# Optimization experiments

Measured on AMD Instinct MI355X. Metric: run time of the kernel, lower is better.

## Reference

```python
import jax, jax.numpy as jnp
import numpy as np
import math

B, S, D, H, R = 4, 2048, 512, 8, 8  # R = k+1 relative slots per direction


def setup_inputs() -> dict:
    key = jax.random.key(0)
    ks = jax.random.split(key, 16)
    dk = D // H
    sc = 1.0 / math.sqrt(D)
    return {
        "query": jax.random.normal(ks[0], (B, S, D), jnp.float32),
        "key": jax.random.normal(ks[1], (B, S, D), jnp.float32),
        "value": jax.random.normal(ks[2], (B, S, D), jnp.float32),
        "start_nodes": jax.random.randint(ks[3], (B, H, R, S), 0, S, jnp.int64 if jax.config.jax_enable_x64 else jnp.int32),
        "end_nodes": jax.random.randint(ks[4], (B, H, R, S), 0, S, jnp.int64 if jax.config.jax_enable_x64 else jnp.int32),
        "rel_q": jax.random.normal(ks[5], (1, H, 2 * R, dk), jnp.float32),
        "rel_k": jax.random.normal(ks[6], (1, H, 2 * R, dk), jnp.float32),
        "rel_v": jax.random.normal(ks[7], (1, H, 2 * R, dk), jnp.float32),
        "Wq": jax.random.normal(ks[8], (D, D), jnp.float32) * sc,
        "bq": jnp.zeros((D,), jnp.float32),
        "Wk": jax.random.normal(ks[9], (D, D), jnp.float32) * sc,
        "bk": jnp.zeros((D,), jnp.float32),
        "Wv": jax.random.normal(ks[10], (D, D), jnp.float32) * sc,
        "bv": jnp.zeros((D,), jnp.float32),
        "Wo": jax.random.normal(ks[11], (D, D), jnp.float32) * sc,
        "bo": jnp.zeros((D,), jnp.float32),
    }


def reference(query, key, value, start_nodes, end_nodes, rel_q, rel_k, rel_v,
              Wq, bq, Wk, bk, Wv, bv, Wo, bo):
    Bs, Ss, Ds = query.shape
    Hs = start_nodes.shape[1]
    dk = Ds // Hs

    def proj(x, W, b):
        return (x @ W.T + b).reshape(Bs, Ss, Hs, dk).transpose(0, 2, 1, 3)  # [B,H,S,dk]

    q = proj(query, Wq, bq)
    k = proj(key, Wk, bk)
    v = proj(value, Wv, bv)

    start_mask = start_nodes == -1
    sn = jnp.where(start_mask, 0, start_nodes)  # -1 padding -> 0 (masked out below)
    qidx = jnp.concatenate([end_nodes, sn], axis=2)  # [B,H,2R,S]
    kidx = jnp.concatenate([sn, end_nodes], axis=2)

    bi = jnp.arange(Bs)[:, None, None, None]
    hi = jnp.arange(Hs)[None, :, None, None]
    q_ctx = q[bi, hi, qidx]  # [B,H,2R,S,dk]
    k_ctx = k[bi, hi, kidx]
    v_ctx = v[bi, hi, kidx]

    # c2c + c2p + p2c, scale_factor = 3 (rel_q and rel_k both provided)
    scores = ((q_ctx * k_ctx).sum(-1)
              + (q_ctx * rel_k[:, :, :, None, :]).sum(-1)
              + (rel_q[:, :, :, None, :] * k_ctx).sum(-1))
    scores = scores / (3.0 * jnp.sqrt(jnp.asarray(dk, scores.dtype)))

    # mask: padded edges masked in both halves; first S flat entries always masked
    mask = jnp.concatenate([start_mask, start_mask], axis=2).reshape(Bs, Hs, -1)
    mask = mask.at[:, :, :Ss].set(True)
    sflat = jnp.exp(jnp.where(mask, -1e9, scores.reshape(Bs, Hs, -1)))  # [B,H,2R*S]

    qf = qidx.reshape(Bs, Hs, -1)
    b2 = jnp.arange(Bs)[:, None, None]
    h2 = jnp.arange(Hs)[None, :, None]
    # scatter-add softmax denominator over destination nodes, then gather back
    denom = jnp.zeros((Bs, Hs, Ss), sflat.dtype).at[b2, h2, qf].add(sflat)
    denom = jnp.where(denom == 0, -1e9, denom)
    probs = (sflat / denom[b2, h2, qf]).reshape(Bs, Hs, -1, Ss, 1)  # [B,H,2R,S,1]

    attn_v = probs * (v_ctx + rel_v[:, :, :, None, :])  # [B,H,2R,S,dk]
    out = jnp.zeros((Bs, Hs, Ss, dk), attn_v.dtype).at[b2, h2, qf].add(
        attn_v.reshape(Bs, Hs, -1, dk))  # scatter-add aggregation over edges

    out = out.transpose(0, 2, 1, 3).reshape(Bs, Ss, Ds)
    return out @ Wo.T + bo
```

## Files before the change

kernel.cpp:

```cpp
#include <hip/hip_runtime.h>
#include <math.h>

#define B_ 4
#define S_ 2048
#define D_ 512
#define H_ 8
#define R_ 8
#define DK_ 64
#define NEDGE (B_*H_*2*R_*S_)
#define EPB   (2*R_*S_)
#define ELLCAP 64

typedef __attribute__((ext_vector_type(8))) short bf16x8;
typedef __attribute__((ext_vector_type(8))) unsigned short ushort8_t;
typedef __attribute__((ext_vector_type(4))) float f32x4;

#define AS1q const __attribute__((address_space(1)))
#define AS3q __attribute__((address_space(3)))

__device__ inline unsigned short f2bf(float f) {
    unsigned u = __builtin_bit_cast(unsigned, f);
    u += 0x7fffu + ((u >> 16) & 1u);
    return (unsigned short)(u >> 16);
}
__device__ inline float bf2f(unsigned short u) {
    return __builtin_bit_cast(float, ((unsigned)u) << 16);
}

__global__ __launch_bounds__(256) void prep(
    const float* __restrict__ query, const float* __restrict__ key,
    const float* __restrict__ value,
    const float* __restrict__ Wq, const float* __restrict__ Wk,
    const float* __restrict__ Wv, const float* __restrict__ Wo,
    const float* __restrict__ rel_q, const float* __restrict__ rel_k,
    const float* __restrict__ rel_v,
    unsigned short* __restrict__ qc, unsigned short* __restrict__ kc,
    unsigned short* __restrict__ vc,
    unsigned short* __restrict__ wqb, unsigned short* __restrict__ wkb,
    unsigned short* __restrict__ wvb, unsigned short* __restrict__ wob,
    unsigned short* __restrict__ rqb, unsigned short* __restrict__ rkb,
    unsigned short* __restrict__ rvb)
{
    int bid = blockIdx.x;
    const float* x;
    unsigned short* y;
    size_t i;
    if (bid < 12288) {
        int z = bid >> 12;
        x = (z == 0) ? query : (z == 1) ? key : value;
        y = (z == 0) ? qc : (z == 1) ? kc : vc;
        i = ((size_t)(bid & 4095) * 256 + threadIdx.x) * 4;
    } else if (bid < 13312) {
        int r = bid - 12288;
        int z = r >> 8;
        x = (z == 0) ? Wq : (z == 1) ? Wk : (z == 2) ? Wv : Wo;
        y = (z == 0) ? wqb : (z == 1) ? wkb : (z == 2) ? wvb : wob;
        i = ((size_t)(r & 255) * 256 + threadIdx.x) * 4;
    } else {
        int r = bid - 13312;
        int z = r >> 3;
        x = (z == 0) ? rel_q : (z == 1) ? rel_k : rel_v;
        y = (z == 0) ? rqb : (z == 1) ? rkb : rvb;
        i = ((size_t)(r & 7) * 256 + threadIdx.x) * 4;
    }
    float4 v = *(const float4*)&x[i];
    *(ushort4*)&y[i] = make_ushort4(f2bf(v.x), f2bf(v.y), f2bf(v.z), f2bf(v.w));
}

template<int TN>
__global__ __launch_bounds__(256) void gemm_bf16(
    const unsigned short* __restrict__ A0, const unsigned short* __restrict__ A1,
    const unsigned short* __restrict__ A2,
    const unsigned short* __restrict__ W0, const unsigned short* __restrict__ W1,
    const unsigned short* __restrict__ W2,
    const float* __restrict__ bi0, const float* __restrict__ bi1, const float* __restrict__ bi2,
    unsigned short* __restrict__ C0, unsigned short* __restrict__ C1,
    unsigned short* __restrict__ C2,
    float* __restrict__ Cf, int a_bhsd)
{
    constexpr int NFR = TN / 32;
    __shared__ unsigned short As[128 * 64];
    __shared__ unsigned short Bs[TN * 64];
    const int z = blockIdx.z;
    const unsigned short* A = (z == 0) ? A0 : (z == 1) ? A1 : A2;
    const unsigned short* W = (z == 0) ? W0 : (z == 1) ? W1 : W2;
    const float* bias        = (z == 0) ? bi0 : (z == 1) ? bi1 : bi2;
    unsigned short* C        = (z == 0) ? C0 : (z == 1) ? C1 : C2;

    const int t    = threadIdx.x;
    const int lane = t & 63;
    const int w    = t >> 6;
    const int wm   = w >> 1, wn = w & 1;
    const int m0   = blockIdx.x * 128;
    const int n0   = blockIdx.y * TN;

    const int lr    = lane >> 3;
    const int cglob = (lane & 7) ^ lr;

    f32x4 acc[4][NFR] = {};

    for (int kk = 0; kk < D_; kk += 64) {
        #pragma unroll
        for (int i = 0; i < 4; ++i) {
            int rowl = w * 32 + i * 8;
            int m = m0 + rowl + lr;
            const unsigned short* ga;
            if (a_bhsd) {
                int b = m >> 11, s = m & (S_ - 1), h = kk >> 6;
                ga = A + ((((size_t)b * H_ + h) * S_ + s) << 6) + cglob * 8;
            } else {
                ga = A + (size_t)m * D_ + kk + cglob * 8;
            }
            __builtin_amdgcn_global_load_lds((AS1q unsigned*)ga,
                (AS3q unsigned*)(As + rowl * 64), 16, 0, 0);
        }
        #pragma unroll
        for (int i = 0; i < TN / 32; ++i) {
            int rowl = w * (TN / 4) + i * 8;
            const unsigned short* gb =
                W + (size_t)(n0 + rowl + lr) * D_ + kk + cglob * 8;
            __builtin_amdgcn_global_load_lds((AS1q unsigned*)gb,
                (AS3q unsigned*)(Bs + rowl * 64), 16, 0, 0);
        }
        __syncthreads();

        #pragma unroll
        for (int ks = 0; ks < 64; ks += 32) {
            const int c0 = ks >> 3;
            bf16x8 af[4], bfr[NFR];
            #pragma unroll
            for (int mi = 0; mi < 4; ++mi) {
                int row = wm * 64 + mi * 16 + (lane & 15);
                int cp  = (c0 + (lane >> 4)) ^ (lane & 7);
                af[mi] = *(const bf16x8*)&As[row * 64 + cp * 8];
            }
            #pragma unroll
            for (int nj = 0; nj < NFR; ++nj) {
                int row = wn * (TN / 2) + nj * 16 + (lane & 15);
                int cp  = (c0 + (lane >> 4)) ^ (lane & 7);
                bfr[nj] = *(const bf16x8*)&Bs[row * 64 + cp * 8];
            }
            #pragma unroll
            for (int mi = 0; mi < 4; ++mi)
                #pragma unroll
                for (int nj = 0; nj < NFR; ++nj)
                    acc[mi][nj] = __builtin_amdgcn_mfma_f32_16x16x32_bf16(af[mi], bfr[nj], acc[mi][nj], 0, 0, 0);
        }
        __syncthreads();
    }

    #pragma unroll
    for (int mi = 0; mi < 4; ++mi) {
        #pragma unroll
        for (int nj = 0; nj < NFR; ++nj) {
            #pragma unroll
            for (int r = 0; r < 4; ++r) {
                int m = m0 + wm * 64 + mi * 16 + (lane >> 4) * 4 + r;
                int n = n0 + wn * (TN / 2) + nj * 16 + (lane & 15);
                float val = acc[mi][nj][r] + bias[n];
                if (Cf) {
                    Cf[(size_t)m * D_ + n] = val;
                } else {
                    int b = m >> 11, s = m & (S_ - 1);
                    int h = n >> 6,  d = n & 63;
                    C[((((size_t)b * H_ + h) * S_ + s) << 6) + d] = f2bf(val);
                }
            }
        }
    }
}

__global__ __launch_bounds__(1024) void attn_fused(
    const unsigned short* __restrict__ q, const unsigned short* __restrict__ k_,
    const unsigned short* __restrict__ v_,
    const unsigned short* __restrict__ rel_q, const unsigned short* __restrict__ rel_k,
    const unsigned short* __restrict__ rel_v,
    const int* __restrict__ start_nodes, const int* __restrict__ end_nodes,
    unsigned short* __restrict__ attn)
{
    __shared__ unsigned short ell[128 * ELLCAP];
    __shared__ int cnt[128];
    const int bi  = blockIdx.x;
    const int xcd = bi & 7;
    const int loc = bi >> 3;
    const int bh  = xcd * 4 + (loc >> 4);
    const int dlo = (loc & 15) << 7;
    const int t   = threadIdx.x;

    if (t < 128) cnt[t] = 0;
    __syncthreads();

    const int base_idx = bh * (R_ * S_);
    for (int f = t; f < EPB; f += 1024) {
        int r2 = f >> 11;
        if (r2 == 0) continue;
        int s = f & (S_ - 1);
        int idx = base_idx + (r2 & 7) * S_ + s;
        int sn = start_nodes[idx];
        if (sn == -1) continue;
        int en = end_nodes[idx];
        int dst = (r2 < R_) ? en : sn;
        unsigned rel = (unsigned)(dst - dlo);
        if (rel < 128u) {
            int ki = (r2 < R_) ? sn : en;
            int pos = atomicAdd(&cnt[rel], 1);
            if (pos < ELLCAP)
                ell[(rel << 6) + pos] = (unsigned short)((r2 << 11) | ki);
        }
    }
    __syncthreads();

    const int w    = t >> 6;
    const int lane = t & 63;
    const int grp  = lane >> 3;
    const int sub  = lane & 7;
    const int h    = bh & 7;
    const size_t node_base = ((size_t)bh << 11);

    for (int dd = 0; dd < 8; ++dd) {
        int dl  = dd * 16 + w;
        int dst = dlo + dl;

        ushort8_t q8 = *(const ushort8_t*)&q[((node_base + dst) << 6) + sub * 8];
        float qv[8];
        #pragma unroll
        for (int i = 0; i < 8; ++i) qv[i] = bf2f(q8[i]);

        int n = cnt[dl];
        if (n > ELLCAP) n = ELLCAP;
        int d_all = (int)ell[(dl << 6) + lane];

        float den = 0.f;
        float o[8] = {};
        #pragma unroll 2
        for (int j = 0; j < n; j += 8) {
            int slot = j + grp;
            int d = __shfl(d_all, slot);
            bool valid = slot < n;
            int ki = d & (S_ - 1);
            int r2 = (d >> 11) & 15;
            ushort8_t k8  = *(const ushort8_t*)&k_  [((node_base + ki) << 6) + sub * 8];
            ushort8_t rk8 = *(const ushort8_t*)&rel_k[(((h << 4) + r2) << 6) + sub * 8];
            ushort8_t rq8 = *(const ushort8_t*)&rel_q[(((h << 4) + r2) << 6) + sub * 8];
            float p = 0.f;
            #pragma unroll
            for (int i = 0; i < 8; ++i)
                p = fmaf(bf2f(k8[i]), qv[i] + bf2f(rq8[i]),
                         fmaf(qv[i], bf2f(rk8[i]), p));
            p += __shfl_xor(p, 1);
            p += __shfl_xor(p, 2);
            p += __shfl_xor(p, 4);
            float sf = valid ? __expf(p * (1.0f / 24.0f)) : 0.f;
            ushort8_t v8  = *(const ushort8_t*)&v_  [((node_base + ki) << 6) + sub * 8];
            ushort8_t rv8 = *(const ushort8_t*)&rel_v[(((h << 4) + r2) << 6) + sub * 8];
            den += sf;
            #pragma unroll
            for (int i = 0; i < 8; ++i)
                o[i] = fmaf(sf, bf2f(v8[i]) + bf2f(rv8[i]), o[i]);
        }
        den += __shfl_xor(den, 8); den += __shfl_xor(den, 16); den += __shfl_xor(den, 32);
        #pragma unroll
        for (int i = 0; i < 8; ++i) {
            o[i] += __shfl_xor(o[i], 8);
            o[i] += __shfl_xor(o[i], 16);
            o[i] += __shfl_xor(o[i], 32);
        }
        if (grp == 0) {
            float inv = (den > 0.f) ? 1.0f / den : 0.f;
            ushort8_t r;
            #pragma unroll
            for (int i = 0; i < 8; ++i) r[i] = f2bf(o[i] * inv);
            *(ushort8_t*)&attn[((node_base + dst) << 6) + sub * 8] = r;
        }
    }
}

extern "C" void kernel_launch(void* const* d_in, const int* in_sizes, int n_in,
                              void* d_out, int out_size, void* d_ws, size_t ws_size,
                              hipStream_t stream) {
    const float* query = (const float*)d_in[0];
    const float* key   = (const float*)d_in[1];
    const float* value = (const float*)d_in[2];
    const int* start_nodes = (const int*)d_in[3];
    const int* end_nodes   = (const int*)d_in[4];
    const float* rel_q = (const float*)d_in[5];
    const float* rel_k = (const float*)d_in[6];
    const float* rel_v = (const float*)d_in[7];
    const float* Wq = (const float*)d_in[8];
    const float* bq = (const float*)d_in[9];
    const float* Wk = (const float*)d_in[10];
    const float* bk = (const float*)d_in[11];
    const float* Wv = (const float*)d_in[12];
    const float* bv = (const float*)d_in[13];
    const float* Wo = (const float*)d_in[14];
    const float* bo = (const float*)d_in[15];
    float* out = (float*)d_out;

    const size_t NQ = (size_t)B_ * H_ * S_ * DK_;
    const size_t NW = (size_t)D_ * D_;
    const size_t NR = (size_t)H_ * 2 * R_ * DK_;
    unsigned short* p = (unsigned short*)d_ws;
    unsigned short* qc = p;            p += NQ;
    unsigned short* kc = p;            p += NQ;
    unsigned short* vc = p;            p += NQ;
    unsigned short* q  = p;            p += NQ;
    unsigned short* k  = p;            p += NQ;
    unsigned short* v  = p;            p += NQ;
    unsigned short* attn = p;          p += NQ;
    unsigned short* wqb = p;           p += NW;
    unsigned short* wkb = p;           p += NW;
    unsigned short* wvb = p;           p += NW;
    unsigned short* wob = p;           p += NW;
    unsigned short* rqb = p;           p += NR;
    unsigned short* rkb = p;           p += NR;
    unsigned short* rvb = p;           p += NR;

    prep<<<13336, 256, 0, stream>>>(query, key, value, Wq, Wk, Wv, Wo,
                                    rel_q, rel_k, rel_v,
                                    qc, kc, vc, wqb, wkb, wvb, wob,
                                    rqb, rkb, rvb);

    dim3 ggrid(B_ * S_ / 128, D_ / 128, 3);
    gemm_bf16<128><<<ggrid, 256, 0, stream>>>(qc, kc, vc, wqb, wkb, wvb, bq, bk, bv,
                                              q, k, v, nullptr, 0);

    attn_fused<<<512, 1024, 0, stream>>>(q, k, v, rqb, rkb, rvb,
                                         start_nodes, end_nodes, attn);

    dim3 ogrid(B_ * S_ / 128, D_ / 64, 1);
    gemm_bf16<64><<<ogrid, 256, 0, stream>>>(attn, attn, attn, wob, wob, wob, bo, bo, bo,
                                             nullptr, nullptr, nullptr, out, 1);
}
```

Before: 217.2 us.

## Precompute per-node relative-position score terms in a separate kernel

Adds a rel_dots kernel that computes q·rel_k and k·rel_q for every node and all 16 relative slots, stores them in fp32 scratch that reuses the qc buffer, and has the attention loop read these scalars instead of recomputing two extra dot products per edge. rel_v is now read directly in fp32, and the edge-bucketing loop loads start/end node pairs as int2 and skips the always-masked first segment up front. This cuts per-edge arithmetic and rel-table loads in the gather loop. In exchange it adds a kernel launch, extra per-edge scattered scalar loads from rqk, and changes precision slightly because the rel terms are no longer rounded to bf16.

```diff
diff --git a/kernel.cpp b/kernel.cpp
--- a/kernel.cpp
+++ b/kernel.cpp
@@ -10,6 +10,7 @@
 #define NEDGE (B_*H_*2*R_*S_)
 #define EPB   (2*R_*S_)
 #define ELLCAP 64
+#define SCALE_ (1.0f/24.0f)
 
 typedef __attribute__((ext_vector_type(8))) short bf16x8;
 typedef __attribute__((ext_vector_type(8))) unsigned short ushort8_t;
@@ -32,14 +33,10 @@
     const float* __restrict__ value,
     const float* __restrict__ Wq, const float* __restrict__ Wk,
     const float* __restrict__ Wv, const float* __restrict__ Wo,
-    const float* __restrict__ rel_q, const float* __restrict__ rel_k,
-    const float* __restrict__ rel_v,
     unsigned short* __restrict__ qc, unsigned short* __restrict__ kc,
     unsigned short* __restrict__ vc,
     unsigned short* __restrict__ wqb, unsigned short* __restrict__ wkb,
-    unsigned short* __restrict__ wvb, unsigned short* __restrict__ wob,
-    unsigned short* __restrict__ rqb, unsigned short* __restrict__ rkb,
-    unsigned short* __restrict__ rvb)
+    unsigned short* __restrict__ wvb, unsigned short* __restrict__ wob)
 {
     int bid = blockIdx.x;
     const float* x;
@@ -50,18 +47,12 @@
         x = (z == 0) ? query : (z == 1) ? key : value;
         y = (z == 0) ? qc : (z == 1) ? kc : vc;
         i = ((size_t)(bid & 4095) * 256 + threadIdx.x) * 4;
-    } else if (bid < 13312) {
+    } else {
         int r = bid - 12288;
         int z = r >> 8;
         x = (z == 0) ? Wq : (z == 1) ? Wk : (z == 2) ? Wv : Wo;
         y = (z == 0) ? wqb : (z == 1) ? wkb : (z == 2) ? wvb : wob;
         i = ((size_t)(r & 255) * 256 + threadIdx.x) * 4;
-    } else {
-        int r = bid - 13312;
-        int z = r >> 3;
-        x = (z == 0) ? rel_q : (z == 1) ? rel_k : rel_v;
-        y = (z == 0) ? rqb : (z == 1) ? rkb : rvb;
-        i = ((size_t)(r & 7) * 256 + threadIdx.x) * 4;
     }
     float4 v = *(const float4*)&x[i];
     *(ushort4*)&y[i] = make_ushort4(f2bf(v.x), f2bf(v.y), f2bf(v.z), f2bf(v.w));
@@ -170,11 +161,62 @@
     }
 }
 
+__global__ __launch_bounds__(256) void rel_dots(
+    const unsigned short* __restrict__ q, const unsigned short* __restrict__ k_,
+    const float* __restrict__ rel_q, const float* __restrict__ rel_k,
+    float* __restrict__ qrk, float* __restrict__ rqk)
+{
+    const int t    = threadIdx.x;
+    const int lane = t & 63;
+    const int sub  = lane & 7;
+    const int grp  = lane >> 3;
+    const int wid  = (blockIdx.x << 2) + (t >> 6);
+    const int n0   = wid << 4;
+    const int h    = (n0 >> 11) & 7;
+
+    float rkv[2][8], rqv[2][8];
+    #pragma unroll
+    for (int pp = 0; pp < 2; ++pp) {
+        const float* a = rel_k + (size_t)(((h << 4) + grp + pp * 8) << 6) + sub * 8;
+        const float* b = rel_q + (size_t)(((h << 4) + grp + pp * 8) << 6) + sub * 8;
+        f32x4 a0 = *(const f32x4*)a, a1 = *(const f32x4*)(a + 4);
+        f32x4 b0 = *(const f32x4*)b, b1 = *(const f32x4*)(b + 4);
+        #pragma unroll
+        for (int i = 0; i < 4; ++i) {
+            rkv[pp][i] = a0[i]; rkv[pp][4 + i] = a1[i];
+            rqv[pp][i] = b0[i]; rqv[pp][4 + i] = b1[i];
+        }
+    }
+    for (int i = 0; i < 16; ++i) {
+        int node = n0 + i;
+        ushort8_t q8 = *(const ushort8_t*)&q [((size_t)node << 6) + sub * 8];
+        ushort8_t k8 = *(const ushort8_t*)&k_[((size_t)node << 6) + sub * 8];
+        float qv[8], kv[8];
+        #pragma unroll
+        for (int e = 0; e < 8; ++e) { qv[e] = bf2f(q8[e]); kv[e] = bf2f(k8[e]); }
+        #pragma unroll
+        for (int pp = 0; pp < 2; ++pp) {
+            float a = 0.f, b = 0.f;
+            #pragma unroll
+            for (int e = 0; e < 8; ++e) {
+                a = fmaf(qv[e], rkv[pp][e], a);
+                b = fmaf(kv[e], rqv[pp][e], b);
+            }
+            a += __shfl_xor(a, 1); a += __shfl_xor(a, 2); a += __shfl_xor(a, 4);
+            b += __shfl_xor(b, 1); b += __shfl_xor(b, 2); b += __shfl_xor(b, 4);
+            if (sub == 0) {
+                qrk[((size_t)node << 4) + grp + pp * 8] = a * SCALE_;
+                rqk[((size_t)node << 4) + grp + pp * 8] = b * SCALE_;
+            }
+        }
+    }
+}
+
 __global__ __launch_bounds__(1024) void attn_fused(
     const unsigned short* __restrict__ q, const unsigned short* __restrict__ k_,
     const unsigned short* __restrict__ v_,
-    const unsigned short* __restrict__ rel_q, const unsigned short* __restrict__ rel_k,
-    const unsigned short* __restrict__ rel_v,
+    const float* __restrict__ qrk, const float* __restrict__ rqk,
+    const float* __restrict__ rel_v,
     const int* __restrict__ start_nodes, const int* __restrict__ end_nodes,
     unsigned short* __restrict__ attn)
 {
@@ -191,21 +233,25 @@
     __syncthreads();
 
     const int base_idx = bh * (R_ * S_);
-    for (int f = t; f < EPB; f += 1024) {
+    for (int f = S_ + t * 2; f < EPB; f += 2048) {
         int r2 = f >> 11;
-        if (r2 == 0) continue;
-        int s = f & (S_ - 1);
-        int idx = base_idx + (r2 & 7) * S_ + s;
-        int sn = start_nodes[idx];
-        if (sn == -1) continue;
-        int en = end_nodes[idx];
-        int dst = (r2 < R_) ? en : sn;
-        unsigned rel = (unsigned)(dst - dlo);
-        if (rel < 128u) {
-            int ki = (r2 < R_) ? sn : en;
-            int pos = atomicAdd(&cnt[rel], 1);
-            if (pos < ELLCAP)
-                ell[(rel << 6) + pos] = (unsigned short)((r2 << 11) | ki);
+        int s  = f & (S_ - 1);
+        int idx = base_idx + ((r2 & 7) << 11) + s;
+        int2 sn2 = *(const int2*)&start_nodes[idx];
+        int2 en2 = *(const int2*)&end_nodes[idx];
+        #pragma unroll
+        for (int u = 0; u < 2; ++u) {
+            int sn = u ? sn2.y : sn2.x;
+            if (sn == -1) continue;
+            int en = u ? en2.y : en2.x;
+            int dst = (r2 < R_) ? en : sn;
+            unsigned rel = (unsigned)(dst - dlo);
+            if (rel < 128u) {
+                int ki = (r2 < R_) ? sn : en;
+                int pos = atomicAdd(&cnt[rel], 1);
+                if (pos < ELLCAP)
+                    ell[(rel << 6) + pos] = (unsigned short)((r2 << 11) | ki);
+            }
         }
     }
     __syncthreads();
@@ -216,6 +262,9 @@
     const int sub  = lane & 7;
     const int h    = bh & 7;
     const size_t node_base = ((size_t)bh << 11);
+    const float* qrk_bh = qrk + (node_base << 4);
+    const float* rqk_bh = rqk + (node_base << 4);
+    const float* rvh    = rel_v + ((size_t)(h << 4) << 6);
 
     for (int dd = 0; dd < 8; ++dd) {
         int dl  = dd * 16 + w;
@@ -225,6 +274,7 @@
         float qv[8];
         #pragma unroll
         for (int i = 0; i < 8; ++i) qv[i] = bf2f(q8[i]);
+        float qrk_l = qrk_bh[((size_t)dst << 4) + (lane & 15)];
 
         int n = cnt[dl];
         if (n > ELLCAP) n = ELLCAP;
@@ -239,24 +289,27 @@
             bool valid = slot < n;
             int ki = d & (S_ - 1);
             int r2 = (d >> 11) & 15;
-            ushort8_t k8  = *(const ushort8_t*)&k_  [((node_base + ki) << 6) + sub * 8];
-            ushort8_t rk8 = *(const ushort8_t*)&rel_k[(((h << 4) + r2) << 6) + sub * 8];
-            ushort8_t rq8 = *(const ushort8_t*)&rel_q[(((h << 4) + r2) << 6) + sub * 8];
+            ushort8_t k8 = *(const ushort8_t*)&k_[((node_base + ki) << 6) + sub * 8];
             float p = 0.f;
             #pragma unroll
             for (int i = 0; i < 8; ++i)
-                p = fmaf(bf2f(k8[i]), qv[i] + bf2f(rq8[i]),
-                         fmaf(qv[i], bf2f(rk8[i]), p));
+                p = fmaf(bf2f(k8[i]), qv[i], p);
             p += __shfl_xor(p, 1);
             p += __shfl_xor(p, 2);
             p += __shfl_xor(p, 4);
-            float sf = valid ? __expf(p * (1.0f / 24.0f)) : 0.f;
-            ushort8_t v8  = *(const ushort8_t*)&v_  [((node_base + ki) << 6) + sub * 8];
-            ushort8_t rv8 = *(const ushort8_t*)&rel_v[(((h << 4) + r2) << 6) + sub * 8];
+            float tb = __shfl(qrk_l, r2) + rqk_bh[((size_t)ki << 4) + r2];
+            float sf = valid ? __expf(fmaf(p, SCALE_, tb)) : 0.f;
+            ushort8_t v8 = *(const ushort8_t*)&v_[((node_base + ki) << 6) + sub * 8];
+            const float* rvp = rvh + (r2 << 6) + sub * 8;
+            f32x4 rv0 = *(const f32x4*)rvp;
+            f32x4 rv1 = *(const f32x4*)(rvp + 4);
             den += sf;
             #pragma unroll
-            for (int i = 0; i < 8; ++i)
-                o[i] = fmaf(sf, bf2f(v8[i]) + bf2f(rv8[i]), o[i]);
+            for (int i = 0; i < 4; ++i)
+                o[i] = fmaf(sf, bf2f(v8[i]) + rv0[i], o[i]);
+            #pragma unroll
+            for (int i = 0; i < 4; ++i)
+                o[4 + i] = fmaf(sf, bf2f(v8[4 + i]) + rv1[i], o[4 + i]);
         }
         den += __shfl_xor(den, 8); den += __shfl_xor(den, 16); den += __shfl_xor(den, 32);
         #pragma unroll
@@ -298,7 +351,6 @@
 
     const size_t NQ = (size_t)B_ * H_ * S_ * DK_;
     const size_t NW = (size_t)D_ * D_;
-    const size_t NR = (size_t)H_ * 2 * R_ * DK_;
     unsigned short* p = (unsigned short*)d_ws;
     unsigned short* qc = p;            p += NQ;
     unsigned short* kc = p;            p += NQ;
@@ -311,20 +363,19 @@
     unsigned short* wkb = p;           p += NW;
     unsigned short* wvb = p;           p += NW;
     unsigned short* wob = p;           p += NW;
-    unsigned short* rqb = p;           p += NR;
-    unsigned short* rkb = p;           p += NR;
-    unsigned short* rvb = p;           p += NR;
-
-    prep<<<13336, 256, 0, stream>>>(query, key, value, Wq, Wk, Wv, Wo,
-                                    rel_q, rel_k, rel_v,
-                                    qc, kc, vc, wqb, wkb, wvb, wob,
-                                    rqb, rkb, rvb);
+    float* qrk = (float*)qc;
+    float* rqk = qrk + ((size_t)1 << 20);
+
+    prep<<<13312, 256, 0, stream>>>(query, key, value, Wq, Wk, Wv, Wo,
+                                    qc, kc, vc, wqb, wkb, wvb, wob);
 
     dim3 ggrid(B_ * S_ / 128, D_ / 128, 3);
     gemm_bf16<128><<<ggrid, 256, 0, stream>>>(qc, kc, vc, wqb, wkb, wvb, bq, bk, bv,
                                               q, k, v, nullptr, 0);
 
-    attn_fused<<<512, 1024, 0, stream>>>(q, k, v, rqb, rkb, rvb,
+    rel_dots<<<1024, 256, 0, stream>>>(q, k, rel_q, rel_k, qrk, rqk);
+
+    attn_fused<<<512, 1024, 0, stream>>>(q, k, v, qrk, rqk, rel_v,
                                          start_nodes, end_nodes, attn);
 
     dim3 ogrid(B_ * S_ / 128, D_ / 64, 1);
```

After: 228.4 us. 1.05x slower.
